# Kernel optimization log

Measured on AMD Instinct MI355X. Metric: run time of the kernel, lower is better.

## Reference

```python
import jax, jax.numpy as jnp
import numpy as np
from jax import lax

B_, T_, C_ = 8, 1024, 768
H_, W_ = 32, 32
N_LAYER, LAYER_ID = 12, 5


def _fancy_init():
    # faithful 'fancy' init from Random_SpatialMix._init_weights
    r01 = LAYER_ID / (N_LAYER - 1)
    r1a0 = 1.0 - LAYER_ID / N_LAYER
    h = np.arange(C_, dtype=np.float64)
    decay = -5 + 8 * (h / (C_ - 1)) ** (0.7 + 1.3 * r01)
    zig = ((np.arange(C_) + 1) % 3 - 1) * 0.5
    first = np.log(0.3) + zig
    xlin = h / C_
    mix_k = xlin ** r1a0
    mix_v = xlin ** r1a0 + 0.3 * r01
    mix_r = xlin ** (0.5 * r1a0)
    f32 = lambda a: jnp.asarray(a, jnp.float32)
    return f32(decay), f32(first), f32(mix_k), f32(mix_v), f32(mix_r)


def setup_inputs() -> dict:
    key = jax.random.key(0)
    ks = jax.random.split(key, 6)
    s = 1.0 / np.sqrt(C_)
    x = jax.random.normal(ks[0], (B_, T_, C_), jnp.float32)
    Wk = jax.random.normal(ks[1], (C_, C_), jnp.float32) * s
    Wv = jax.random.normal(ks[2], (C_, C_), jnp.float32) * s
    Wr = jax.random.normal(ks[3], (C_, C_), jnp.float32) * s
    Wo = jax.random.normal(ks[4], (C_, C_), jnp.float32) * s
    decay, first, mk, mv, mr = _fancy_init()
    perm = jax.random.permutation(ks[5], C_).astype(jnp.int32)
    return dict(x=x, w_key=Wk, w_value=Wv, w_receptance=Wr, w_output=Wo,
                spatial_decay=decay, spatial_first=first,
                mix_k=mk, mix_v=mv, mix_r=mr, perm=perm, H=H_, W=W_)


def _shift2d(a, dh, dw, H, W):
    # zero-padded 2D shift of [B,H,W,g]
    pad = [(0, 0), (max(dh, 0), max(-dh, 0)), (max(dw, 0), max(-dw, 0)), (0, 0)]
    a = jnp.pad(a, pad)
    return a[:, max(-dh, 0):max(-dh, 0) + H, max(-dw, 0):max(-dw, 0) + W, :]


def q_shift(x, H, W, shift_pixel=1, gamma=0.25):
    # VRWKV q_shift: 4 channel groups shifted right/left/down/up, rest copied
    B, T, C = x.shape
    xi = x.reshape(B, H, W, C)
    g = int(C * gamma)
    parts = [
        _shift2d(xi[..., 0:g], 0, shift_pixel, H, W),
        _shift2d(xi[..., g:2 * g], 0, -shift_pixel, H, W),
        _shift2d(xi[..., 2 * g:3 * g], shift_pixel, 0, H, W),
        _shift2d(xi[..., 3 * g:4 * g], -shift_pixel, 0, H, W),
        xi[..., 4 * g:],
    ]
    return jnp.concatenate(parts, axis=-1).reshape(B, T, C)


def wkv(w, u, k, v):
    # RWKV-v4 WKV kernel (numerically stable form). w,u: [C]; k,v: [B,T,C]
    w = -jnp.exp(w)  # kernel applies w = -exp(w)
    B, T, C = k.shape

    def step(carry, kv):
        a, b, p = carry  # each [B,C]
        kt, vt = kv
        q = jnp.maximum(p, u + kt)
        e1 = jnp.exp(p - q)
        e2 = jnp.exp(u + kt - q)
        y = (e1 * a + e2 * vt) / (e1 * b + e2)
        q2 = jnp.maximum(p + w, kt)
        e1 = jnp.exp(p + w - q2)
        e2 = jnp.exp(kt - q2)
        return (e1 * a + e2 * vt, e1 * b + e2, q2), y

    init = (jnp.zeros((B, C), k.dtype), jnp.zeros((B, C), k.dtype),
            jnp.full((B, C), -1e38, k.dtype))
    _, y = lax.scan(step, init, (jnp.moveaxis(k, 1, 0), jnp.moveaxis(v, 1, 0)))
    return jnp.moveaxis(y, 0, 1)


def reference(x, w_key, w_value, w_receptance, w_output,
              spatial_decay, spatial_first, mix_k, mix_v, mix_r, perm, H, W):
    B, T, C = x.shape
    xx = q_shift(x, H, W)
    xk = x * mix_k + xx * (1 - mix_k)
    xv = x * mix_v + xx * (1 - mix_v)
    xr = x * mix_r + xx * (1 - mix_r)
    k = xk @ w_key.T
    v = xv @ w_value.T
    sr = jax.nn.sigmoid(xr @ w_receptance.T)
    # training path: shuffle CHANNEL axis (RevShuffle dim=2), run WKV, reverse
    ks_ = k[:, :, perm]
    vs_ = v[:, :, perm]
    wkv_s = wkv(spatial_decay / T, spatial_first / T, ks_, vs_)
    rev = jnp.zeros_like(perm).at[perm].set(jnp.arange(C, dtype=perm.dtype))
    wkv_out = wkv_s[:, :, rev]
    return (sr * wkv_out) @ w_output.T
```

## Files before the change

### kernel.cpp

```cpp
#include <hip/hip_runtime.h>
#include <hip/hip_bf16.h>
#include <stdint.h>

#define B_N 8
#define T_N 1024
#define C_N 768
#define M_N (B_N*T_N)
#define NCH 32
#define LCH (T_N/NCH)
#define BK32 32
#define KS  (C_N/BK32)

typedef __attribute__((ext_vector_type(4))) float f32x4;
typedef __attribute__((ext_vector_type(8))) short s16x8;
typedef __attribute__((ext_vector_type(4))) unsigned short u16x4;

__device__ __forceinline__ unsigned short f2bf(float f){
  unsigned int u = __float_as_uint(f);
  u += 0x7FFFu + ((u >> 16) & 1u);
  return (unsigned short)(u >> 16);
}
__device__ __forceinline__ float bf2f(unsigned short h){
  return __uint_as_float(((unsigned int)h) << 16);
}

__device__ __forceinline__ void async16(const unsigned short* g, unsigned short* l){
  __builtin_amdgcn_global_load_lds(
      (const __attribute__((address_space(1))) unsigned int*)g,
      (__attribute__((address_space(3))) unsigned int*)l, 16, 0, 0);
}

__global__ __launch_bounds__(256) void prep_weights(
    const float* __restrict__ Wk, const float* __restrict__ Wv,
    const float* __restrict__ Wr, const float* __restrict__ Wo,
    const int* __restrict__ perm,
    unsigned short* __restrict__ Wall,
    unsigned short* __restrict__ Wop)
{
  int idx = blockIdx.x*256 + threadIdx.x;
  int r = idx / C_N, c = idx - r*C_N;
  int pr = perm[r];
  Wall[idx]            = f2bf(Wk[pr*C_N + c]);
  Wall[idx +   (size_t)C_N*C_N] = f2bf(Wv[pr*C_N + c]);
  Wall[idx + 2*(size_t)C_N*C_N] = f2bf(Wr[pr*C_N + c]);
  Wop[idx] = f2bf(Wo[r*C_N + perm[c]]);
}

__global__ __launch_bounds__(256) void mix_kernel(
    const float* __restrict__ x,
    const float* __restrict__ mk, const float* __restrict__ mv, const float* __restrict__ mr,
    unsigned short* __restrict__ xk, unsigned short* __restrict__ xv, unsigned short* __restrict__ xr)
{
  int idx = blockIdx.x*256 + threadIdx.x;
  int n  = idx / (C_N/4);
  int c4 = (idx - n*(C_N/4)) * 4;
  int t = n & (T_N-1);
  int h = t >> 5, w = t & 31;
  int grp = c4 / 192;
  int dh = (grp==2) ? -1 : (grp==3) ? 1 : 0;
  int dw = (grp==0) ? -1 : (grp==1) ? 1 : 0;
  int h2 = h + dh, w2 = w + dw;
  bool valid = ((unsigned)h2 < 32u) && ((unsigned)w2 < 32u);
  f32x4 xc = *(const f32x4*)(x + (size_t)n*C_N + c4);
  f32x4 xx = {0.f,0.f,0.f,0.f};
  if (valid) xx = *(const f32x4*)(x + (size_t)(n + dh*32 + dw)*C_N + c4);
  f32x4 vk = *(const f32x4*)(mk + c4);
  f32x4 vv = *(const f32x4*)(mv + c4);
  f32x4 vr = *(const f32x4*)(mr + c4);
  u16x4 ok, ov, orr;
  #pragma unroll
  for (int i=0;i<4;++i){
    float d = xc[i] - xx[i];
    ok[i]  = f2bf(xx[i] + vk[i]*d);
    ov[i]  = f2bf(xx[i] + vv[i]*d);
    orr[i] = f2bf(xx[i] + vr[i]*d);
  }
  *(u16x4*)(xk + (size_t)n*C_N + c4) = ok;
  *(u16x4*)(xv + (size_t)n*C_N + c4) = ov;
  *(u16x4*)(xr + (size_t)n*C_N + c4) = orr;
}

__global__ __launch_bounds__(256, 3) void gemm_kvr(
    const unsigned short* __restrict__ xk, const unsigned short* __restrict__ xv,
    const unsigned short* __restrict__ xr,
    const unsigned short* __restrict__ Wall,
    unsigned short* __restrict__ kb, unsigned short* __restrict__ vb,
    unsigned short* __restrict__ srb)
{
  int flat = blockIdx.y * gridDim.x + blockIdx.x;
  int swz  = (flat & 7) * 144 + (flat >> 3);
  const int mb = swz / 18, nb = swz - 18*mb;
  const int m0 = mb * 128;
  const int n0 = nb * 128;
  const int z  = nb / 6;
  const unsigned short* A = (z==0)? xk : (z==1)? xv : xr;

  __shared__ __align__(16) unsigned short As[3][128*BK32];
  __shared__ __align__(16) unsigned short Bs[3][128*BK32];
  const int tid = threadIdx.x;
  const int lane = tid & 63, wid = tid >> 6;
  const int wr = wid >> 1, wc = wid & 1;
  f32x4 acc[4][4];
  #pragma unroll
  for (int i=0;i<4;++i)
    #pragma unroll
    for (int j=0;j<4;++j) acc[i][j] = (f32x4){0.f,0.f,0.f,0.f};

  const int sgcol = ((lane & 3) ^ ((lane >> 3) & 3)) * 8;
  const int srow  = lane >> 2;
  const int lr  = lane & 15;
  const int kh  = lane >> 4;
  const int phys = (kh ^ ((lr >> 1) & 3)) * 8;

  auto stage = [&](int buf, int k0){
    #pragma unroll
    for (int i=0;i<2;++i){
      int rbase = i*64 + wid*16;
      async16(&A   [(size_t)(m0 + rbase + srow)*C_N + k0 + sgcol], &As[buf][rbase*BK32]);
      async16(&Wall[(size_t)(n0 + rbase + srow)*C_N + k0 + sgcol], &Bs[buf][rbase*BK32]);
    }
  };

  auto compute = [&](int buf){
    s16x8 af[4], bfr[4];
    #pragma unroll
    for (int mi=0;mi<4;++mi) af[mi]  = *(const s16x8*)&As[buf][(wr*64 + mi*16 + lr)*BK32 + phys];
    #pragma unroll
    for (int ni=0;ni<4;++ni) bfr[ni] = *(const s16x8*)&Bs[buf][(wc*64 + ni*16 + lr)*BK32 + phys];
    __builtin_amdgcn_s_setprio(1);
    #pragma unroll
    for (int mi=0;mi<4;++mi)
      #pragma unroll
      for (int ni=0;ni<4;++ni)
        acc[mi][ni] = __builtin_amdgcn_mfma_f32_16x16x32_bf16(af[mi], bfr[ni], acc[mi][ni], 0,0,0);
    __builtin_amdgcn_s_setprio(0);
  };

  stage(0, 0);
  stage(1, BK32);
  #pragma unroll 1
  for (int t = 0; t < KS; ++t){
    if (t + 2 < KS) stage((t+2)%3, (t+2)*BK32);
    if (t + 2 < KS)      asm volatile("s_waitcnt vmcnt(8)" ::: "memory");
    else if (t + 1 < KS) asm volatile("s_waitcnt vmcnt(4)" ::: "memory");
    else                 asm volatile("s_waitcnt vmcnt(0)" ::: "memory");
    __builtin_amdgcn_s_barrier();
    compute(t%3);
    __builtin_amdgcn_s_barrier();
  }

  const int lr4 = (lane>>4)*4, lc = lane & 15;
  const int colbase = n0 - z*C_N;
  #pragma unroll
  for (int mi=0;mi<4;++mi){
    #pragma unroll
    for (int ni=0;ni<4;++ni){
      #pragma unroll
      for (int i=0;i<4;++i){
        int m = m0 + wr*64 + mi*16 + lr4 + i;
        int n = colbase + wc*64 + ni*16 + lc;
        float val = acc[mi][ni][i];
        if (z==0)      kb[(size_t)m*C_N + n] = f2bf(val);
        else if (z==1) vb[(size_t)m*C_N + n] = f2bf(val);
        else           srb[(size_t)m*C_N + n] = f2bf(1.f/(1.f + __expf(-val)));
      }
    }
  }
}

__global__ __launch_bounds__(256, 3) void gemm_out(
    const unsigned short* __restrict__ A, const unsigned short* __restrict__ Bw,
    float* __restrict__ out)
{
  int flat = blockIdx.y * gridDim.x + blockIdx.x;
  int swz  = (flat & 7) * 48 + (flat >> 3);
  const int mb = swz / 6, nb = swz - 6*mb;
  const int m0 = mb*128, n0 = nb*128;
  __shared__ __align__(16) unsigned short As[3][128*BK32];
  __shared__ __align__(16) unsigned short Bs[3][128*BK32];
  const int tid = threadIdx.x;
  const int lane = tid & 63, wid = tid >> 6;
  const int wr = wid >> 1, wc = wid & 1;
  f32x4 acc[4][4];
  #pragma unroll
  for (int i=0;i<4;++i)
    #pragma unroll
    for (int j=0;j<4;++j) acc[i][j] = (f32x4){0.f,0.f,0.f,0.f};

  const int sgcol = ((lane & 3) ^ ((lane >> 3) & 3)) * 8;
  const int srow  = lane >> 2;
  const int lr  = lane & 15;
  const int kh  = lane >> 4;
  const int phys = (kh ^ ((lr >> 1) & 3)) * 8;

  auto stage = [&](int buf, int k0){
    #pragma unroll
    for (int i=0;i<2;++i){
      int rbase = i*64 + wid*16;
      async16(&A [(size_t)(m0 + rbase + srow)*C_N + k0 + sgcol], &As[buf][rbase*BK32]);
      async16(&Bw[(size_t)(n0 + rbase + srow)*C_N + k0 + sgcol], &Bs[buf][rbase*BK32]);
    }
  };

  auto compute = [&](int buf){
    s16x8 af[4], bfr[4];
    #pragma unroll
    for (int mi=0;mi<4;++mi) af[mi]  = *(const s16x8*)&As[buf][(wr*64 + mi*16 + lr)*BK32 + phys];
    #pragma unroll
    for (int ni=0;ni<4;++ni) bfr[ni] = *(const s16x8*)&Bs[buf][(wc*64 + ni*16 + lr)*BK32 + phys];
    __builtin_amdgcn_s_setprio(1);
    #pragma unroll
    for (int mi=0;mi<4;++mi)
      #pragma unroll
      for (int ni=0;ni<4;++ni)
        acc[mi][ni] = __builtin_amdgcn_mfma_f32_16x16x32_bf16(af[mi], bfr[ni], acc[mi][ni], 0,0,0);
    __builtin_amdgcn_s_setprio(0);
  };

  stage(0, 0);
  stage(1, BK32);
  #pragma unroll 1
  for (int t = 0; t < KS; ++t){
    if (t + 2 < KS) stage((t+2)%3, (t+2)*BK32);
    if (t + 2 < KS)      asm volatile("s_waitcnt vmcnt(8)" ::: "memory");
    else if (t + 1 < KS) asm volatile("s_waitcnt vmcnt(4)" ::: "memory");
    else                 asm volatile("s_waitcnt vmcnt(0)" ::: "memory");
    __builtin_amdgcn_s_barrier();
    compute(t%3);
    __builtin_amdgcn_s_barrier();
  }

  const int lr4 = (lane>>4)*4, lc = lane & 15;
  #pragma unroll
  for (int mi=0;mi<4;++mi)
    #pragma unroll
    for (int ni=0;ni<4;++ni)
      #pragma unroll
      for (int i=0;i<4;++i){
        int m = m0 + wr*64 + mi*16 + lr4 + i;
        int n = n0 + wc*64 + ni*16 + lc;
        out[(size_t)m*C_N + n] = acc[mi][ni][i];
      }
}

__global__ __launch_bounds__(256) void wkv_phase1(
    const unsigned short* __restrict__ kb, const unsigned short* __restrict__ vb,
    const float* __restrict__ decay,
    float* __restrict__ sa, float* __restrict__ sb, float* __restrict__ sp)
{
  int g = blockIdx.x*256 + threadIdx.x;
  int j = g % C_N;
  int cb = g / C_N;
  int b = cb % B_N, c = cb / B_N;
  float w = -__expf(decay[j] * (1.0f/T_N));
  float a = 0.f, bb = 0.f, p = -1e38f;
  size_t base = ((size_t)b*T_N + c*LCH)*C_N + j;
  #pragma unroll 4
  for (int t = 0; t < LCH; ++t){
    size_t o = base + (size_t)t*C_N;
    float kt = bf2f(kb[o]), vt = bf2f(vb[o]);
    float pw = p + w;
    float q2 = fmaxf(pw, kt);
    float e1 = __expf(pw - q2), e2 = __expf(kt - q2);
    a  = e1*a + e2*vt;
    bb = e1*bb + e2;
    p  = q2;
  }
  sa[g] = a; sb[g] = bb; sp[g] = p;
}

__global__ __launch_bounds__(256) void wkv_phase2(
    const float* __restrict__ decay,
    float* __restrict__ sa, float* __restrict__ sb, float* __restrict__ sp)
{
  int g = blockIdx.x*256 + threadIdx.x;
  int j = g % C_N, b = g / C_N;
  float w = -__expf(decay[j] * (1.0f/T_N));
  float wL = w * (float)LCH;
  float a = 0.f, bb = 0.f, p = -1e38f;
  for (int c = 0; c < NCH; ++c){
    size_t idx = ((size_t)c*B_N + b)*C_N + j;
    float la = sa[idx], lb = sb[idx], lp = sp[idx];
    sa[idx] = a; sb[idx] = bb; sp[idx] = p;
    float p1 = p + wL;
    float pn = fmaxf(p1, lp);
    float e1 = __expf(p1 - pn), e2 = __expf(lp - pn);
    a  = e1*a + e2*la;
    bb = e1*bb + e2*lb;
    p  = pn;
  }
}

__global__ __launch_bounds__(256) void wkv_phase3(
    const unsigned short* __restrict__ kb, const unsigned short* __restrict__ vb,
    const unsigned short* __restrict__ srb,
    const float* __restrict__ decay, const float* __restrict__ first,
    const float* __restrict__ sa, const float* __restrict__ sb,
    const float* __restrict__ sp,
    unsigned short* __restrict__ zp)
{
  int g = blockIdx.x*256 + threadIdx.x;
  int j = g % C_N;
  int cb = g / C_N;
  int b = cb % B_N, c = cb / B_N;
  float w = -__expf(decay[j] * (1.0f/T_N));
  float u = first[j] * (1.0f/T_N);
  float a = sa[g], bb = sb[g], p = sp[g];
  size_t base = ((size_t)b*T_N + c*LCH)*C_N + j;
  #pragma unroll 2
  for (int t = 0; t < LCH; ++t){
    size_t o = base + (size_t)t*C_N;
    float kt = bf2f(kb[o]), vt = bf2f(vb[o]);
    float uk = u + kt;
    float q  = fmaxf(p, uk);
    float e1 = __expf(p - q), e2 = __expf(uk - q);
    float y  = __fdividef(e1*a + e2*vt, e1*bb + e2);
    zp[o] = f2bf(bf2f(srb[o]) * y);
    float pw = p + w;
    float q2 = fmaxf(pw, kt);
    float e1b = __expf(pw - q2), e2b = __expf(kt - q2);
    a  = e1b*a + e2b*vt;
    bb = e1b*bb + e2b;
    p  = q2;
  }
}

extern "C" void kernel_launch(void* const* d_in, const int* in_sizes, int n_in,
                              void* d_out, int out_size, void* d_ws, size_t ws_size,
                              hipStream_t stream)
{
  const float* x     = (const float*)d_in[0];
  const float* Wk    = (const float*)d_in[1];
  const float* Wv    = (const float*)d_in[2];
  const float* Wr    = (const float*)d_in[3];
  const float* Wo    = (const float*)d_in[4];
  const float* decay = (const float*)d_in[5];
  const float* first = (const float*)d_in[6];
  const float* mk    = (const float*)d_in[7];
  const float* mv    = (const float*)d_in[8];
  const float* mr    = (const float*)d_in[9];
  const int*   perm  = (const int*)d_in[10];
  float* out = (float*)d_out;

  char* ws = (char*)d_ws;
  size_t off = 0;
  auto alloc = [&](size_t bytes)->char* {
    char* p = ws + off;
    off += (bytes + 255) & ~(size_t)255;
    return p;
  };
  const size_t MC = (size_t)M_N * C_N;
  const size_t CC = (size_t)C_N * C_N;
  const size_t SC = (size_t)NCH * B_N * C_N;
  unsigned short* xk   = (unsigned short*)alloc(MC*2);
  unsigned short* xv   = (unsigned short*)alloc(MC*2);
  unsigned short* xr   = (unsigned short*)alloc(MC*2);
  unsigned short* zp   = (unsigned short*)alloc(MC*2);
  unsigned short* Wall = (unsigned short*)alloc(CC*3*2);
  unsigned short* Wop  = (unsigned short*)alloc(CC*2);
  unsigned short* srb  = (unsigned short*)alloc(MC*2);
  unsigned short* kb   = (unsigned short*)alloc(MC*2);
  unsigned short* vb   = (unsigned short*)alloc(MC*2);
  float* sa  = (float*)alloc(SC*4);
  float* sb  = (float*)alloc(SC*4);
  float* sp  = (float*)alloc(SC*4);

  prep_weights<<<dim3(CC/256), dim3(256), 0, stream>>>(Wk, Wv, Wr, Wo, perm,
                                                       Wall, Wop);
  mix_kernel<<<dim3(MC/4/256), dim3(256), 0, stream>>>(x, mk, mv, mr, xk, xv, xr);
  gemm_kvr<<<dim3(M_N/128, 3*C_N/128), dim3(256), 0, stream>>>(
      xk, xv, xr, Wall, kb, vb, srb);
  wkv_phase1<<<dim3(SC/256), dim3(256), 0, stream>>>(kb, vb, decay, sa, sb, sp);
  wkv_phase2<<<dim3(B_N*C_N/256), dim3(256), 0, stream>>>(decay, sa, sb, sp);
  wkv_phase3<<<dim3(SC/256), dim3(256), 0, stream>>>(kb, vb, srb, decay, first,
                                                     sa, sb, sp, zp);
  gemm_out<<<dim3(M_N/128, C_N/128), dim3(256), 0, stream>>>(zp, Wop, out);
}
```

Measured before the change: 117.2 us.

## Merge prep kernels, retile GEMM block mapping, stage epilogue via LDS

Folds the weight-prep and token-mix kernels into one launch, with block ranges choosing the role, to save a launch and let the two overlap. It changes the XCD block swizzle in both GEMMs so each XCD works on 8 consecutive M tiles across all N tiles, aiming for better L2 reuse of A rows. The gemm_kvr epilogue now writes bf16 results into a padded LDS tile that reuses the operand buffers, then stores 16-byte vectors instead of scattered 2-byte global writes. The cost is an extra barrier and LDS round trip in the epilogue.

After: 109.7 us. 1.07x faster.

```diff
diff --git a/kernel.cpp b/kernel.cpp
--- a/kernel.cpp
+++ b/kernel.cpp
@@ -30,28 +30,27 @@
       (__attribute__((address_space(3))) unsigned int*)l, 16, 0, 0);
 }
 
-__global__ __launch_bounds__(256) void prep_weights(
+__global__ __launch_bounds__(256) void prep_mix(
+    const float* __restrict__ x,
     const float* __restrict__ Wk, const float* __restrict__ Wv,
     const float* __restrict__ Wr, const float* __restrict__ Wo,
     const int* __restrict__ perm,
-    unsigned short* __restrict__ Wall,
-    unsigned short* __restrict__ Wop)
-{
-  int idx = blockIdx.x*256 + threadIdx.x;
-  int r = idx / C_N, c = idx - r*C_N;
-  int pr = perm[r];
-  Wall[idx]            = f2bf(Wk[pr*C_N + c]);
-  Wall[idx +   (size_t)C_N*C_N] = f2bf(Wv[pr*C_N + c]);
-  Wall[idx + 2*(size_t)C_N*C_N] = f2bf(Wr[pr*C_N + c]);
-  Wop[idx] = f2bf(Wo[r*C_N + perm[c]]);
-}
-
-__global__ __launch_bounds__(256) void mix_kernel(
-    const float* __restrict__ x,
     const float* __restrict__ mk, const float* __restrict__ mv, const float* __restrict__ mr,
-    unsigned short* __restrict__ xk, unsigned short* __restrict__ xv, unsigned short* __restrict__ xr)
-{
-  int idx = blockIdx.x*256 + threadIdx.x;
+    unsigned short* __restrict__ Wall, unsigned short* __restrict__ Wop,
+    unsigned short* __restrict__ xk, unsigned short* __restrict__ xv,
+    unsigned short* __restrict__ xr)
+{
+  if (blockIdx.x < 2304){
+    int idx = blockIdx.x*256 + threadIdx.x;
+    int r = idx / C_N, c = idx - r*C_N;
+    int pr = perm[r];
+    Wall[idx]                     = f2bf(Wk[pr*C_N + c]);
+    Wall[idx +   (size_t)C_N*C_N] = f2bf(Wv[pr*C_N + c]);
+    Wall[idx + 2*(size_t)C_N*C_N] = f2bf(Wr[pr*C_N + c]);
+    Wop[idx] = f2bf(Wo[r*C_N + perm[c]]);
+    return;
+  }
+  int idx = (blockIdx.x - 2304)*256 + threadIdx.x;
   int n  = idx / (C_N/4);
   int c4 = (idx - n*(C_N/4)) * 4;
   int t = n & (T_N-1);
@@ -88,15 +87,18 @@
     unsigned short* __restrict__ srb)
 {
   int flat = blockIdx.y * gridDim.x + blockIdx.x;
-  int swz  = (flat & 7) * 144 + (flat >> 3);
-  const int mb = swz / 18, nb = swz - 18*mb;
+  const int xcd = flat & 7, q = flat >> 3;
+  const int mb = xcd*8 + (q & 7);
+  const int nb = q >> 3;
   const int m0 = mb * 128;
   const int n0 = nb * 128;
   const int z  = nb / 6;
   const unsigned short* A = (z==0)? xk : (z==1)? xv : xr;
 
-  __shared__ __align__(16) unsigned short As[3][128*BK32];
-  __shared__ __align__(16) unsigned short Bs[3][128*BK32];
+  __shared__ union {
+    struct { unsigned short As[3][128*BK32]; unsigned short Bs[3][128*BK32]; } s;
+    unsigned short ct[128*132];
+  } u;
   const int tid = threadIdx.x;
   const int lane = tid & 63, wid = tid >> 6;
   const int wr = wid >> 1, wc = wid & 1;
@@ -116,17 +118,17 @@
     #pragma unroll
     for (int i=0;i<2;++i){
       int rbase = i*64 + wid*16;
-      async16(&A   [(size_t)(m0 + rbase + srow)*C_N + k0 + sgcol], &As[buf][rbase*BK32]);
-      async16(&Wall[(size_t)(n0 + rbase + srow)*C_N + k0 + sgcol], &Bs[buf][rbase*BK32]);
+      async16(&A   [(size_t)(m0 + rbase + srow)*C_N + k0 + sgcol], &u.s.As[buf][rbase*BK32]);
+      async16(&Wall[(size_t)(n0 + rbase + srow)*C_N + k0 + sgcol], &u.s.Bs[buf][rbase*BK32]);
     }
   };
 
   auto compute = [&](int buf){
     s16x8 af[4], bfr[4];
     #pragma unroll
-    for (int mi=0;mi<4;++mi) af[mi]  = *(const s16x8*)&As[buf][(wr*64 + mi*16 + lr)*BK32 + phys];
-    #pragma unroll
-    for (int ni=0;ni<4;++ni) bfr[ni] = *(const s16x8*)&Bs[buf][(wc*64 + ni*16 + lr)*BK32 + phys];
+    for (int mi=0;mi<4;++mi) af[mi]  = *(const s16x8*)&u.s.As[buf][(wr*64 + mi*16 + lr)*BK32 + phys];
+    #pragma unroll
+    for (int ni=0;ni<4;++ni) bfr[ni] = *(const s16x8*)&u.s.Bs[buf][(wc*64 + ni*16 + lr)*BK32 + phys];
     __builtin_amdgcn_s_setprio(1);
     #pragma unroll
     for (int mi=0;mi<4;++mi)
@@ -149,22 +151,30 @@
     __builtin_amdgcn_s_barrier();
   }
 
+  unsigned short* dst = (z==0)? kb : (z==1)? vb : srb;
+  const int colbase = n0 - z*C_N;
   const int lr4 = (lane>>4)*4, lc = lane & 15;
-  const int colbase = n0 - z*C_N;
   #pragma unroll
   for (int mi=0;mi<4;++mi){
     #pragma unroll
     for (int ni=0;ni<4;++ni){
       #pragma unroll
       for (int i=0;i<4;++i){
-        int m = m0 + wr*64 + mi*16 + lr4 + i;
-        int n = colbase + wc*64 + ni*16 + lc;
+        int r  = wr*64 + mi*16 + lr4 + i;
+        int cc = wc*64 + ni*16 + lc;
         float val = acc[mi][ni][i];
-        if (z==0)      kb[(size_t)m*C_N + n] = f2bf(val);
-        else if (z==1) vb[(size_t)m*C_N + n] = f2bf(val);
-        else           srb[(size_t)m*C_N + n] = f2bf(1.f/(1.f + __expf(-val)));
+        if (z==2) val = 1.f/(1.f + __expf(-val));
+        u.ct[r*132 + cc] = f2bf(val);
       }
     }
+  }
+  __builtin_amdgcn_s_barrier();
+  #pragma unroll
+  for (int p=0;p<8;++p){
+    int f = (p*256 + tid)*8;
+    int r = f >> 7, cc = f & 127;
+    s16x8 v8 = *(const s16x8*)&u.ct[r*132 + cc];
+    *(s16x8*)&dst[(size_t)(m0+r)*C_N + colbase + cc] = v8;
   }
 }
 
@@ -173,8 +183,9 @@
     float* __restrict__ out)
 {
   int flat = blockIdx.y * gridDim.x + blockIdx.x;
-  int swz  = (flat & 7) * 48 + (flat >> 3);
-  const int mb = swz / 6, nb = swz - 6*mb;
+  const int xcd = flat & 7, q = flat >> 3;
+  const int mb = xcd*8 + (q & 7);
+  const int nb = q >> 3;
   const int m0 = mb*128, n0 = nb*128;
   __shared__ __align__(16) unsigned short As[3][128*BK32];
   __shared__ __align__(16) unsigned short Bs[3][128*BK32];
@@ -365,9 +376,8 @@
   float* sb  = (float*)alloc(SC*4);
   float* sp  = (float*)alloc(SC*4);
 
-  prep_weights<<<dim3(CC/256), dim3(256), 0, stream>>>(Wk, Wv, Wr, Wo, perm,
-                                                       Wall, Wop);
-  mix_kernel<<<dim3(MC/4/256), dim3(256), 0, stream>>>(x, mk, mv, mr, xk, xv, xr);
+  prep_mix<<<dim3(2304 + 6144), dim3(256), 0, stream>>>(
+      x, Wk, Wv, Wr, Wo, perm, mk, mv, mr, Wall, Wop, xk, xv, xr);
   gemm_kvr<<<dim3(M_N/128, 3*C_N/128), dim3(256), 0, stream>>>(
       xk, xv, xr, Wall, kb, vb, srb);
   wkv_phase1<<<dim3(SC/256), dim3(256), 0, stream>>>(kb, vb, decay, sa, sb, sp);
```
